# Kernel tuning notes

Measured on AMD Instinct MI355X. Metric: run time of the kernel, lower is better.

Reference implementation:

```python
import jax, jax.numpy as jnp
import numpy as np
import math

B_SZ, T, D_IN, D_OUT, N = 8, 4096, 256, 256, 512
RMIN, RMAX, MAX_PHASE = 0.99, 1.0, 6.283


def setup_inputs() -> dict:
    key = jax.random.key(0)
    ks = jax.random.split(key, 8)
    u_in = jax.random.normal(ks[0], (B_SZ, T, D_IN), dtype=jnp.float32)
    u1 = jax.random.uniform(ks[1], (N,), dtype=jnp.float32)
    u2 = jax.random.uniform(ks[2], (N,), dtype=jnp.float32)
    # LRU parametrization from 'Resurrecting Linear Recurrences'
    nu_log = jnp.log(-0.5 * jnp.log(u1 * (RMAX + RMIN) * (RMAX - RMIN) + RMIN ** 2))
    theta_log = jnp.log(MAX_PHASE * u2)
    lambda_mod = jnp.exp(-jnp.exp(nu_log))
    gamma_log = jnp.log(jnp.sqrt(1.0 - jnp.square(lambda_mod)))
    B_real = jax.random.normal(ks[3], (N, D_IN), dtype=jnp.float32) / math.sqrt(2 * D_IN)
    B_imag = jax.random.normal(ks[4], (N, D_IN), dtype=jnp.float32) / math.sqrt(2 * D_IN)
    C_real = jax.random.normal(ks[5], (D_OUT, N), dtype=jnp.float32) / math.sqrt(N)
    C_imag = jax.random.normal(ks[6], (D_OUT, N), dtype=jnp.float32) / math.sqrt(N)
    D = jax.random.normal(ks[7], (D_OUT, D_IN), dtype=jnp.float32) / math.sqrt(D_IN)
    return {"u_in": u_in, "nu_log": nu_log, "theta_log": theta_log,
            "gamma_log": gamma_log, "B_real": B_real, "B_imag": B_imag,
            "C_real": C_real, "C_imag": C_imag, "D": D}


def _lru_forward(u_in, nu_log, theta_log, gamma_log, B_real, B_imag, C_real, C_imag, D):
    lambda_mod = jnp.exp(-jnp.exp(nu_log))
    theta = jnp.exp(theta_log)
    lam = (lambda_mod * jnp.cos(theta) + 1j * lambda_mod * jnp.sin(theta)).astype(jnp.complex64)  # [N]
    gammas = jnp.exp(gamma_log)
    Bc = (B_real + 1j * B_imag).astype(jnp.complex64)  # [N, D_in]
    Cc = (C_real + 1j * C_imag).astype(jnp.complex64)  # [D_out, N]
    # driving term: gamma * (u_t @ B^T)  -> [b, t, n]
    Bu = gammas.astype(jnp.complex64) * jnp.einsum('bti,ni->btn', u_in.astype(jnp.complex64), Bc)
    # linear recurrence x_t = lam * x_{t-1} + Bu_t, x_0 prior = 0, via associative scan
    a = jnp.broadcast_to(lam, Bu.shape)

    def combine(e1, e2):
        a1, b1 = e1
        a2, b2 = e2
        return a1 * a2, a2 * b1 + b2

    _, x = jax.lax.associative_scan(combine, (a, Bu), axis=1)  # [b, t, n] complex
    y = 2.0 * jnp.real(jnp.einsum('btn,on->bto', x, Cc)) + jnp.einsum('bti,oi->bto', u_in, D)
    return y


def reference(u_in, nu_log, theta_log, gamma_log, B_real, B_imag, C_real, C_imag, D):
    return _lru_forward(u_in, nu_log, theta_log, gamma_log, B_real, B_imag, C_real, C_imag, D)
```

## Files before the change

### kernel.cpp

```cpp
#include <hip/hip_runtime.h>
#include <hip/hip_bf16.h>
#include <math.h>

#define B_SZ    8
#define T_LEN   4096
#define DIN     256
#define DOUT    256
#define NST     512
#define M_ROWS  (B_SZ * T_LEN)
#define N1      (2 * NST)
#define K2      (N1 + DIN)
#define CHL     128
#define NCH     (T_LEN / CHL)

typedef __attribute__((ext_vector_type(8))) short bf16x8;
typedef __attribute__((ext_vector_type(4))) float f32x4;
typedef __hip_bfloat16 bf16;

#define OFF_UBF  67108864
#define OFF_WP   83886080
#define OFF_W2   84410368
#define OFF_LAM  85065728
#define OFF_LAML 85069824
#define OFF_SSUM 85073920

__device__ __forceinline__ void gl_lds16(const bf16* g, bf16* l) {
    __builtin_amdgcn_global_load_lds(
        (const __attribute__((address_space(1))) void*)g,
        (__attribute__((address_space(3))) void*)l, 16, 0, 0);
}

__global__ __launch_bounds__(256) void prep(const float* __restrict__ u,
        const float* __restrict__ nu_log, const float* __restrict__ theta_log,
        const float* __restrict__ gamma_log,
        const float* __restrict__ B_real, const float* __restrict__ B_imag,
        const float* __restrict__ C_real, const float* __restrict__ C_imag,
        const float* __restrict__ Dm,
        bf16* __restrict__ ub, bf16* __restrict__ Wp, bf16* __restrict__ W2,
        float* __restrict__ lam, float* __restrict__ lamL) {
    int bid = blockIdx.x, tid = threadIdx.x;
    if (bid < 8192) {
        int i = bid * 256 + tid;
        float4 v = ((const float4*)u)[i];
        union { bf16 h[4]; uint2 u2; } p;
        p.h[0] = __float2bfloat16(v.x); p.h[1] = __float2bfloat16(v.y);
        p.h[2] = __float2bfloat16(v.z); p.h[3] = __float2bfloat16(v.w);
        ((uint2*)ub)[i] = p.u2;
    } else if (bid < 9216) {
        int c = bid - 8192;
        int n = c & (NST - 1);
        float g = expf(gamma_log[n]);
        const float* src = (c < NST) ? (B_real + (size_t)n * DIN)
                                     : (B_imag + (size_t)n * DIN);
        Wp[(size_t)c * DIN + tid] = __float2bfloat16(g * src[tid]);
        int idx = c * 256 + tid;
        if (idx < NST) {
            float lm = expf(-expf(nu_log[idx]));
            float th = expf(theta_log[idx]);
            float lr = lm * cosf(th), li = lm * sinf(th);
            lam[idx] = lr; lam[NST + idx] = li;
            float ar = lr, ai = li;
#pragma unroll
            for (int q = 0; q < 7; ++q) {
                float nr = ar * ar - ai * ai;
                float ni = 2.f * ar * ai;
                ar = nr; ai = ni;
            }
            lamL[idx] = ar; lamL[NST + idx] = ai;
        }
    } else {
        int idx = (bid - 9216) * 256 + tid;
        if (idx < DOUT * K2) {
            int o = idx / K2, c = idx - o * K2;
            float v;
            if (c < NST)            v =  2.0f * C_real[(size_t)o * NST + c];
            else if (c < 2 * NST)   v = -2.0f * C_imag[(size_t)o * NST + (c - NST)];
            else                    v =  Dm[(size_t)o * DIN + (c - 2 * NST)];
            W2[idx] = __float2bfloat16(v);
        }
    }
}

__global__ __launch_bounds__(256) void gemm1(const bf16* __restrict__ u,
                                             const bf16* __restrict__ Wp,
                                             bf16* __restrict__ Bu) {
    __shared__ bf16 As[128 * 32];
    __shared__ bf16 Bs[128 * 32];
    __shared__ bf16 Cs[128 * 136];
    const int tid = threadIdx.x;
    const int m0 = blockIdx.x * 128, n0 = blockIdx.y * 128;
    const int lane = tid & 63, w = tid >> 6;
    const int wm = (w >> 1) * 64, wn = (w & 1) * 64;
    const int lr16 = lane & 15, kq = (lane >> 4) * 8;
    const int srow = tid >> 2, scol = (tid & 3) * 8;

    f32x4 acc[4][4] = {};
    for (int k0 = 0; k0 < DIN; k0 += 32) {
        gl_lds16(u  + (size_t)(m0 + srow) * DIN + k0 + scol,       &As[tid * 8]);
        gl_lds16(u  + (size_t)(m0 + 64 + srow) * DIN + k0 + scol,  &As[2048 + tid * 8]);
        gl_lds16(Wp + (size_t)(n0 + srow) * DIN + k0 + scol,       &Bs[tid * 8]);
        gl_lds16(Wp + (size_t)(n0 + 64 + srow) * DIN + k0 + scol,  &Bs[2048 + tid * 8]);
        __syncthreads();
        bf16x8 af[4], bfr[4];
#pragma unroll
        for (int i = 0; i < 4; ++i)
            af[i] = *(const bf16x8*)(&As[(wm + i * 16 + lr16) * 32 + kq]);
#pragma unroll
        for (int j = 0; j < 4; ++j)
            bfr[j] = *(const bf16x8*)(&Bs[(wn + j * 16 + lr16) * 32 + kq]);
#pragma unroll
        for (int i = 0; i < 4; ++i)
#pragma unroll
            for (int j = 0; j < 4; ++j)
                acc[i][j] = __builtin_amdgcn_mfma_f32_16x16x32_bf16(af[i], bfr[j], acc[i][j], 0, 0, 0);
        __syncthreads();
    }
    const int crow = (lane >> 4) * 4, ccol = lane & 15;
#pragma unroll
    for (int i = 0; i < 4; ++i)
#pragma unroll
        for (int j = 0; j < 4; ++j)
#pragma unroll
            for (int r = 0; r < 4; ++r)
                Cs[(wm + i * 16 + crow + r) * 136 + wn + j * 16 + ccol] =
                    __float2bfloat16(acc[i][j][r]);
    __syncthreads();
#pragma unroll
    for (int p = 0; p < 8; ++p) {
        int row = p * 16 + (tid >> 4);
        int colg = (tid & 15) * 8;
        *(uint4*)(&Bu[(size_t)(m0 + row) * N1 + n0 + colg]) =
            *(const uint4*)(&Cs[row * 136 + colg]);
    }
}

__global__ __launch_bounds__(512) void scan1(const bf16* __restrict__ Bu,
                                             const float* __restrict__ lam,
                                             float* __restrict__ Ssum) {
    int n = threadIdx.x;
    int c = blockIdx.x;
    int b = blockIdx.y;
    float lr = lam[n], li = lam[NST + n];
    const bf16* base = Bu + ((size_t)b * T_LEN + (size_t)c * CHL) * N1;
    float sr = 0.f, si = 0.f;
    for (int j = 0; j < CHL; ++j) {
        float br = __bfloat162float(base[(size_t)j * N1 + n]);
        float bi = __bfloat162float(base[(size_t)j * N1 + NST + n]);
        float tr = lr * sr - li * si + br;
        float ti = lr * si + li * sr + bi;
        sr = tr; si = ti;
    }
    size_t o = ((size_t)b * NCH + c) * N1 + n;
    Ssum[o] = sr; Ssum[o + NST] = si;
}

__global__ __launch_bounds__(512) void scan3(bf16* __restrict__ Bu,
                                             const float* __restrict__ lam,
                                             const float* __restrict__ lamL,
                                             const float* __restrict__ Ssum) {
    int n = threadIdx.x, c = blockIdx.x, b = blockIdx.y;
    float lr = lam[n], li = lam[NST + n];
    float Lr = lamL[n], Li = lamL[NST + n];
    float pr = 0.f, pi = 0.f;
    for (int cp = 0; cp < c; ++cp) {
        size_t o = ((size_t)b * NCH + cp) * N1 + n;
        float sr = Ssum[o], si = Ssum[o + NST];
        float tr = Lr * pr - Li * pi + sr;
        float ti = Lr * pi + Li * pr + si;
        pr = tr; pi = ti;
    }
    float xr = pr, xi = pi;
    bf16* base = Bu + ((size_t)b * T_LEN + (size_t)c * CHL) * N1;
    for (int j = 0; j < CHL; ++j) {
        float br = __bfloat162float(base[(size_t)j * N1 + n]);
        float bi = __bfloat162float(base[(size_t)j * N1 + NST + n]);
        float tr = lr * xr - li * xi + br;
        float ti = lr * xi + li * xr + bi;
        xr = tr; xi = ti;
        base[(size_t)j * N1 + n]       = __float2bfloat16(xr);
        base[(size_t)j * N1 + NST + n] = __float2bfloat16(xi);
    }
}

__global__ __launch_bounds__(512) void gemm2(const bf16* __restrict__ X,
                                             const bf16* __restrict__ u,
                                             const bf16* __restrict__ W2,
                                             float* __restrict__ y) {
    __shared__ bf16 As[128 * 32];
    __shared__ bf16 Bs[128 * 32];
    const int tid = threadIdx.x;
    const int m0 = blockIdx.x * 128, n0 = blockIdx.y * 128;
    const int lane = tid & 63, w = tid >> 6;
    const int wm = (w >> 2) * 64, wn = (w & 3) * 32;
    const int lr16 = lane & 15, kq = (lane >> 4) * 8;
    const int srow = tid >> 2, scol = (tid & 3) * 8;

    f32x4 acc[4][2] = {};
    for (int k0 = 0; k0 < K2; k0 += 32) {
        const bf16* Asrc; size_t lda; int kc;
        if (k0 < N1) { Asrc = X; lda = N1;  kc = k0; }
        else         { Asrc = u; lda = DIN; kc = k0 - N1; }
        gl_lds16(Asrc + (size_t)(m0 + srow) * lda + kc + scol, &As[tid * 8]);
        gl_lds16(W2 + (size_t)(n0 + srow) * K2 + k0 + scol,    &Bs[tid * 8]);
        __syncthreads();
        bf16x8 af[4], bfr[2];
#pragma unroll
        for (int i = 0; i < 4; ++i)
            af[i] = *(const bf16x8*)(&As[(wm + i * 16 + lr16) * 32 + kq]);
#pragma unroll
        for (int j = 0; j < 2; ++j)
            bfr[j] = *(const bf16x8*)(&Bs[(wn + j * 16 + lr16) * 32 + kq]);
#pragma unroll
        for (int i = 0; i < 4; ++i)
#pragma unroll
            for (int j = 0; j < 2; ++j)
                acc[i][j] = __builtin_amdgcn_mfma_f32_16x16x32_bf16(af[i], bfr[j], acc[i][j], 0, 0, 0);
        __syncthreads();
    }
    const int crow = (lane >> 4) * 4, ccol = lane & 15;
#pragma unroll
    for (int i = 0; i < 4; ++i)
#pragma unroll
        for (int j = 0; j < 2; ++j)
#pragma unroll
            for (int r = 0; r < 4; ++r)
                y[(size_t)(m0 + wm + i * 16 + crow + r) * DOUT + n0 + wn + j * 16 + ccol] = acc[i][j][r];
}

extern "C" void kernel_launch(void* const* d_in, const int* in_sizes, int n_in,
                              void* d_out, int out_size, void* d_ws, size_t ws_size,
                              hipStream_t stream) {
    const float* u_in      = (const float*)d_in[0];
    const float* nu_log    = (const float*)d_in[1];
    const float* theta_log = (const float*)d_in[2];
    const float* gamma_log = (const float*)d_in[3];
    const float* B_real    = (const float*)d_in[4];
    const float* B_imag    = (const float*)d_in[5];
    const float* C_real    = (const float*)d_in[6];
    const float* C_imag    = (const float*)d_in[7];
    const float* Dm        = (const float*)d_in[8];
    float* y = (float*)d_out;
    char* ws = (char*)d_ws;

    bf16*  Bu   = (bf16*)ws;
    bf16*  u_bf = (bf16*)(ws + OFF_UBF);
    bf16*  Wp   = (bf16*)(ws + OFF_WP);
    bf16*  W2   = (bf16*)(ws + OFF_W2);
    float* lam  = (float*)(ws + OFF_LAM);
    float* lamL = (float*)(ws + OFF_LAML);
    float* Ssum = (float*)(ws + OFF_SSUM);

    prep<<<10496, 256, 0, stream>>>(u_in, nu_log, theta_log, gamma_log,
                                    B_real, B_imag, C_real, C_imag, Dm,
                                    u_bf, Wp, W2, lam, lamL);
    gemm1<<<dim3(M_ROWS / 128, N1 / 128), 256, 0, stream>>>(u_bf, Wp, Bu);
    scan1<<<dim3(NCH, B_SZ), 512, 0, stream>>>(Bu, lam, Ssum);
    scan3<<<dim3(NCH, B_SZ), 512, 0, stream>>>(Bu, lam, lamL, Ssum);
    gemm2<<<dim3(M_ROWS / 128, DOUT / 128), 512, 0, stream>>>(Bu, u_bf, W2, y);
}
```

Measured before the change: 198.8 us.

## Fuse chunk-scan fixup with output GEMM, keeping states in LDS

Merges the second scan pass and the output projection GEMM into one kernel. Each block scans its 128-step chunk in two halves of 64 rows, writes the bf16 states into shared memory, and then multiplies them against W2 (plus the u/D part) directly. This removes the write-back of X to global memory and its re-read by a separate GEMM. The cost is that the fused grid has only 256 blocks and large LDS use (~140KB), and the serial scan phase now alternates with the MFMA phase inside each block, which may reduce parallelism and latency hiding.

```diff
diff --git a/kernel.cpp b/kernel.cpp
--- a/kernel.cpp
+++ b/kernel.cpp
@@ -12,6 +12,7 @@
 #define K2      (N1 + DIN)
 #define CHL     128
 #define NCH     (T_LEN / CHL)
+#define XW      1032
 
 typedef __attribute__((ext_vector_type(8))) short bf16x8;
 typedef __attribute__((ext_vector_type(4))) float f32x4;
@@ -154,77 +155,110 @@
     Ssum[o] = sr; Ssum[o + NST] = si;
 }
 
-__global__ __launch_bounds__(512) void scan3(bf16* __restrict__ Bu,
-                                             const float* __restrict__ lam,
-                                             const float* __restrict__ lamL,
-                                             const float* __restrict__ Ssum) {
-    int n = threadIdx.x, c = blockIdx.x, b = blockIdx.y;
+__global__ __launch_bounds__(512, 2) void scan_gemm2(
+        const bf16* __restrict__ Bu, const bf16* __restrict__ u,
+        const bf16* __restrict__ W2, const float* __restrict__ lam,
+        const float* __restrict__ lamL, const float* __restrict__ Ssum,
+        float* __restrict__ y) {
+    __shared__ bf16 Xs[64 * XW];
+    __shared__ bf16 Bs[256 * 32];
+    const int tid = threadIdx.x;
+    const int c = blockIdx.x, b = blockIdx.y;
+    const int n = tid;
+
     float lr = lam[n], li = lam[NST + n];
     float Lr = lamL[n], Li = lamL[NST + n];
-    float pr = 0.f, pi = 0.f;
+    float xr = 0.f, xi = 0.f;
     for (int cp = 0; cp < c; ++cp) {
         size_t o = ((size_t)b * NCH + cp) * N1 + n;
         float sr = Ssum[o], si = Ssum[o + NST];
-        float tr = Lr * pr - Li * pi + sr;
-        float ti = Lr * pi + Li * pr + si;
-        pr = tr; pi = ti;
-    }
-    float xr = pr, xi = pi;
-    bf16* base = Bu + ((size_t)b * T_LEN + (size_t)c * CHL) * N1;
-    for (int j = 0; j < CHL; ++j) {
-        float br = __bfloat162float(base[(size_t)j * N1 + n]);
-        float bi = __bfloat162float(base[(size_t)j * N1 + NST + n]);
-        float tr = lr * xr - li * xi + br;
-        float ti = lr * xi + li * xr + bi;
+        float tr = Lr * xr - Li * xi + sr;
+        float ti = Lr * xi + Li * xr + si;
         xr = tr; xi = ti;
-        base[(size_t)j * N1 + n]       = __float2bfloat16(xr);
-        base[(size_t)j * N1 + NST + n] = __float2bfloat16(xi);
-    }
-}
-
-__global__ __launch_bounds__(512) void gemm2(const bf16* __restrict__ X,
-                                             const bf16* __restrict__ u,
-                                             const bf16* __restrict__ W2,
-                                             float* __restrict__ y) {
-    __shared__ bf16 As[128 * 32];
-    __shared__ bf16 Bs[128 * 32];
-    const int tid = threadIdx.x;
-    const int m0 = blockIdx.x * 128, n0 = blockIdx.y * 128;
+    }
+
+    const bf16* base = Bu + ((size_t)b * T_LEN + (size_t)c * CHL) * N1;
+    const int row0 = b * T_LEN + c * CHL;
     const int lane = tid & 63, w = tid >> 6;
-    const int wm = (w >> 2) * 64, wn = (w & 3) * 32;
+    const int wn = w * 32;
     const int lr16 = lane & 15, kq = (lane >> 4) * 8;
-    const int srow = tid >> 2, scol = (tid & 3) * 8;
-
-    f32x4 acc[4][2] = {};
-    for (int k0 = 0; k0 < K2; k0 += 32) {
-        const bf16* Asrc; size_t lda; int kc;
-        if (k0 < N1) { Asrc = X; lda = N1;  kc = k0; }
-        else         { Asrc = u; lda = DIN; kc = k0 - N1; }
-        gl_lds16(Asrc + (size_t)(m0 + srow) * lda + kc + scol, &As[tid * 8]);
-        gl_lds16(W2 + (size_t)(n0 + srow) * K2 + k0 + scol,    &Bs[tid * 8]);
+    const int urow = tid >> 3, ucol = (tid & 7) * 32;
+    const int brow = tid >> 1, bcol = (tid & 1) * 16;
+    const int crow = (lane >> 4) * 4, ccol = lane & 15;
+
+    for (int half = 0; half < 2; ++half) {
+        for (int j = 0; j < 64; ++j) {
+            int jj = half * 64 + j;
+            float br = __bfloat162float(base[(size_t)jj * N1 + n]);
+            float bi = __bfloat162float(base[(size_t)jj * N1 + NST + n]);
+            float tr = lr * xr - li * xi + br;
+            float ti = lr * xi + li * xr + bi;
+            xr = tr; xi = ti;
+            Xs[j * XW + n]       = __float2bfloat16(xr);
+            Xs[j * XW + NST + n] = __float2bfloat16(xi);
+        }
+        const bf16* up = u + (size_t)(row0 + half * 64 + urow) * DIN + ucol;
+        uint4 ur0 = *(const uint4*)(up);
+        uint4 ur1 = *(const uint4*)(up + 8);
+        uint4 ur2 = *(const uint4*)(up + 16);
+        uint4 ur3 = *(const uint4*)(up + 24);
+        {
+            int ch0 = w * 2, ch1 = w * 2 + 1;
+            int rr0 = ch0 * 16 + (lane >> 2), rr1 = ch1 * 16 + (lane >> 2);
+            int cb = (lane & 3) * 8;
+            gl_lds16(W2 + (size_t)rr0 * K2 + cb, &Bs[ch0 * 512 + lane * 8]);
+            gl_lds16(W2 + (size_t)rr1 * K2 + cb, &Bs[ch1 * 512 + lane * 8]);
+        }
         __syncthreads();
-        bf16x8 af[4], bfr[2];
+
+        f32x4 acc[4][2] = {};
+        for (int p = 0; p < 40; ++p) {
+            uint4 r0, r1;
+            const bool havep = (p + 1) < 40;
+            if (havep) {
+                int pn = p + 1;
+                int k0g = pn < 32 ? pn * 32 : 1024 + (pn - 32) * 32;
+                const bf16* wp2 = W2 + (size_t)brow * K2 + k0g + bcol;
+                r0 = *(const uint4*)(wp2);
+                r1 = *(const uint4*)(wp2 + 8);
+            }
+            int ca0 = p < 32 ? p * 32 : (p - 32) * 32;
+            bf16x8 af[4], bfr[2];
+#pragma unroll
+            for (int i = 0; i < 4; ++i)
+                af[i] = *(const bf16x8*)(&Xs[(i * 16 + lr16) * XW + ca0 + kq]);
+#pragma unroll
+            for (int j = 0; j < 2; ++j)
+                bfr[j] = *(const bf16x8*)(&Bs[(wn + j * 16 + lr16) * 32 + kq]);
+#pragma unroll
+            for (int i = 0; i < 4; ++i)
+#pragma unroll
+                for (int j = 0; j < 2; ++j)
+                    acc[i][j] = __builtin_amdgcn_mfma_f32_16x16x32_bf16(af[i], bfr[j], acc[i][j], 0, 0, 0);
+            __syncthreads();
+            if (p == 31) {
+                bf16* xd = &Xs[urow * XW + ucol];
+                *(uint4*)(xd)      = ur0;
+                *(uint4*)(xd + 8)  = ur1;
+                *(uint4*)(xd + 16) = ur2;
+                *(uint4*)(xd + 24) = ur3;
+            }
+            if (havep) {
+                bf16* bd = &Bs[brow * 32 + bcol];
+                *(uint4*)(bd)     = r0;
+                *(uint4*)(bd + 8) = r1;
+            }
+            __syncthreads();
+        }
 #pragma unroll
         for (int i = 0; i < 4; ++i)
-            af[i] = *(const bf16x8*)(&As[(wm + i * 16 + lr16) * 32 + kq]);
-#pragma unroll
-        for (int j = 0; j < 2; ++j)
-            bfr[j] = *(const bf16x8*)(&Bs[(wn + j * 16 + lr16) * 32 + kq]);
-#pragma unroll
-        for (int i = 0; i < 4; ++i)
 #pragma unroll
             for (int j = 0; j < 2; ++j)
-                acc[i][j] = __builtin_amdgcn_mfma_f32_16x16x32_bf16(af[i], bfr[j], acc[i][j], 0, 0, 0);
-        __syncthreads();
-    }
-    const int crow = (lane >> 4) * 4, ccol = lane & 15;
-#pragma unroll
-    for (int i = 0; i < 4; ++i)
-#pragma unroll
-        for (int j = 0; j < 2; ++j)
-#pragma unroll
-            for (int r = 0; r < 4; ++r)
-                y[(size_t)(m0 + wm + i * 16 + crow + r) * DOUT + n0 + wn + j * 16 + ccol] = acc[i][j][r];
+#pragma unroll
+                for (int r = 0; r < 4; ++r)
+                    y[(size_t)(row0 + half * 64 + i * 16 + crow + r) * DOUT + wn + j * 16 + ccol] =
+                        acc[i][j][r];
+    }
 }
 
 extern "C" void kernel_launch(void* const* d_in, const int* in_sizes, int n_in,
@@ -255,6 +289,5 @@
                                     u_bf, Wp, W2, lam, lamL);
     gemm1<<<dim3(M_ROWS / 128, N1 / 128), 256, 0, stream>>>(u_bf, Wp, Bu);
     scan1<<<dim3(NCH, B_SZ), 512, 0, stream>>>(Bu, lam, Ssum);
-    scan3<<<dim3(NCH, B_SZ), 512, 0, stream>>>(Bu, lam, lamL, Ssum);
-    gemm2<<<dim3(M_ROWS / 128, DOUT / 128), 512, 0, stream>>>(Bu, u_bf, W2, y);
-}
+    scan_gemm2<<<dim3(NCH, B_SZ), 512, 0, stream>>>(Bu, u_bf, W2, lam, lamL, Ssum, y);
+}
```

Measured after the change: 212.6 us. +7.0%, slower.

## Double-buffer LDS tiles in both GEMMs to overlap global loads with MFMA

Applied to the files above, without the earlier changes.

Both GEMM kernels now use two LDS stages for their A/B tiles. The tile for the next K step is issued into the alternate buffer before the current tile's MFMAs run, so global-to-LDS transfer latency can overlap with compute. In gemm1 the epilogue staging buffer is unioned with the double-buffered tiles, which keeps shared memory per block from growing and may even reduce it. In gemm2 shared memory usage doubles, which could lower occupancy, and the per-iteration barrier still forces the prefetch to complete each step, which limits how much overlap is possible.

```diff
diff --git a/kernel.cpp b/kernel.cpp
--- a/kernel.cpp
+++ b/kernel.cpp
@@ -84,9 +84,10 @@
 __global__ __launch_bounds__(256) void gemm1(const bf16* __restrict__ u,
                                              const bf16* __restrict__ Wp,
                                              bf16* __restrict__ Bu) {
-    __shared__ bf16 As[128 * 32];
-    __shared__ bf16 Bs[128 * 32];
-    __shared__ bf16 Cs[128 * 136];
+    __shared__ union {
+        bf16 ab[2][2][128 * 32];
+        bf16 cs[128 * 136];
+    } sm;
     const int tid = threadIdx.x;
     const int m0 = blockIdx.x * 128, n0 = blockIdx.y * 128;
     const int lane = tid & 63, w = tid >> 6;
@@ -95,19 +96,29 @@
     const int srow = tid >> 2, scol = (tid & 3) * 8;
 
     f32x4 acc[4][4] = {};
-    for (int k0 = 0; k0 < DIN; k0 += 32) {
-        gl_lds16(u  + (size_t)(m0 + srow) * DIN + k0 + scol,       &As[tid * 8]);
-        gl_lds16(u  + (size_t)(m0 + 64 + srow) * DIN + k0 + scol,  &As[2048 + tid * 8]);
-        gl_lds16(Wp + (size_t)(n0 + srow) * DIN + k0 + scol,       &Bs[tid * 8]);
-        gl_lds16(Wp + (size_t)(n0 + 64 + srow) * DIN + k0 + scol,  &Bs[2048 + tid * 8]);
-        __syncthreads();
+    {
+        gl_lds16(u  + (size_t)(m0 + srow) * DIN + scol,       &sm.ab[0][0][tid * 8]);
+        gl_lds16(u  + (size_t)(m0 + 64 + srow) * DIN + scol,  &sm.ab[0][0][2048 + tid * 8]);
+        gl_lds16(Wp + (size_t)(n0 + srow) * DIN + scol,       &sm.ab[0][1][tid * 8]);
+        gl_lds16(Wp + (size_t)(n0 + 64 + srow) * DIN + scol,  &sm.ab[0][1][2048 + tid * 8]);
+    }
+    __syncthreads();
+    for (int t = 0; t < 8; ++t) {
+        const int cur = t & 1;
+        if (t < 7) {
+            int k0 = (t + 1) * 32;
+            gl_lds16(u  + (size_t)(m0 + srow) * DIN + k0 + scol,       &sm.ab[cur ^ 1][0][tid * 8]);
+            gl_lds16(u  + (size_t)(m0 + 64 + srow) * DIN + k0 + scol,  &sm.ab[cur ^ 1][0][2048 + tid * 8]);
+            gl_lds16(Wp + (size_t)(n0 + srow) * DIN + k0 + scol,       &sm.ab[cur ^ 1][1][tid * 8]);
+            gl_lds16(Wp + (size_t)(n0 + 64 + srow) * DIN + k0 + scol,  &sm.ab[cur ^ 1][1][2048 + tid * 8]);
+        }
         bf16x8 af[4], bfr[4];
 #pragma unroll
         for (int i = 0; i < 4; ++i)
-            af[i] = *(const bf16x8*)(&As[(wm + i * 16 + lr16) * 32 + kq]);
+            af[i] = *(const bf16x8*)(&sm.ab[cur][0][(wm + i * 16 + lr16) * 32 + kq]);
 #pragma unroll
         for (int j = 0; j < 4; ++j)
-            bfr[j] = *(const bf16x8*)(&Bs[(wn + j * 16 + lr16) * 32 + kq]);
+            bfr[j] = *(const bf16x8*)(&sm.ab[cur][1][(wn + j * 16 + lr16) * 32 + kq]);
 #pragma unroll
         for (int i = 0; i < 4; ++i)
 #pragma unroll
@@ -122,7 +133,7 @@
         for (int j = 0; j < 4; ++j)
 #pragma unroll
             for (int r = 0; r < 4; ++r)
-                Cs[(wm + i * 16 + crow + r) * 136 + wn + j * 16 + ccol] =
+                sm.cs[(wm + i * 16 + crow + r) * 136 + wn + j * 16 + ccol] =
                     __float2bfloat16(acc[i][j][r]);
     __syncthreads();
 #pragma unroll
@@ -130,7 +141,7 @@
         int row = p * 16 + (tid >> 4);
         int colg = (tid & 15) * 8;
         *(uint4*)(&Bu[(size_t)(m0 + row) * N1 + n0 + colg]) =
-            *(const uint4*)(&Cs[row * 136 + colg]);
+            *(const uint4*)(&sm.cs[row * 136 + colg]);
     }
 }
 
@@ -186,8 +197,7 @@
                                              const bf16* __restrict__ u,
                                              const bf16* __restrict__ W2,
                                              float* __restrict__ y) {
-    __shared__ bf16 As[128 * 32];
-    __shared__ bf16 Bs[128 * 32];
+    __shared__ bf16 ab[2][2][128 * 32];
     const int tid = threadIdx.x;
     const int m0 = blockIdx.x * 128, n0 = blockIdx.y * 128;
     const int lane = tid & 63, w = tid >> 6;
@@ -196,20 +206,26 @@
     const int srow = tid >> 2, scol = (tid & 3) * 8;
 
     f32x4 acc[4][2] = {};
-    for (int k0 = 0; k0 < K2; k0 += 32) {
-        const bf16* Asrc; size_t lda; int kc;
-        if (k0 < N1) { Asrc = X; lda = N1;  kc = k0; }
-        else         { Asrc = u; lda = DIN; kc = k0 - N1; }
-        gl_lds16(Asrc + (size_t)(m0 + srow) * lda + kc + scol, &As[tid * 8]);
-        gl_lds16(W2 + (size_t)(n0 + srow) * K2 + k0 + scol,    &Bs[tid * 8]);
-        __syncthreads();
+    gl_lds16(X  + (size_t)(m0 + srow) * N1 + scol,  &ab[0][0][tid * 8]);
+    gl_lds16(W2 + (size_t)(n0 + srow) * K2 + scol,  &ab[0][1][tid * 8]);
+    __syncthreads();
+    for (int t = 0; t < 40; ++t) {
+        const int cur = t & 1;
+        if (t < 39) {
+            int k0 = (t + 1) * 32;
+            const bf16* Asrc; size_t lda; int kc;
+            if (k0 < N1) { Asrc = X; lda = N1;  kc = k0; }
+            else         { Asrc = u; lda = DIN; kc = k0 - N1; }
+            gl_lds16(Asrc + (size_t)(m0 + srow) * lda + kc + scol, &ab[cur ^ 1][0][tid * 8]);
+            gl_lds16(W2 + (size_t)(n0 + srow) * K2 + k0 + scol,    &ab[cur ^ 1][1][tid * 8]);
+        }
         bf16x8 af[4], bfr[2];
 #pragma unroll
         for (int i = 0; i < 4; ++i)
-            af[i] = *(const bf16x8*)(&As[(wm + i * 16 + lr16) * 32 + kq]);
+            af[i] = *(const bf16x8*)(&ab[cur][0][(wm + i * 16 + lr16) * 32 + kq]);
 #pragma unroll
         for (int j = 0; j < 2; ++j)
-            bfr[j] = *(const bf16x8*)(&Bs[(wn + j * 16 + lr16) * 32 + kq]);
+            bfr[j] = *(const bf16x8*)(&ab[cur][1][(wn + j * 16 + lr16) * 32 + kq]);
 #pragma unroll
         for (int i = 0; i < 4; ++i)
 #pragma unroll
```

After: 193.0 us. -2.9%, faster.
